# Kernel optimization log

Measured on AMD Instinct MI355X. Metric: run time of the kernel, lower is better.

Reference implementation:

```python
import jax, jax.numpy as jnp
import numpy as np

EMBED_DIM = 384
HIDDEN_DIM = 512
CODEBOOK_SIZE = 256
NUM_QUANTIZERS = 4
COMMIT_WEIGHT = 0.25
BATCH = 65536


def setup_inputs() -> dict:
    key = jax.random.key(0)
    ks = jax.random.split(key, 10)
    s_in = 1.0 / np.sqrt(EMBED_DIM)
    s_h = 1.0 / np.sqrt(HIDDEN_DIM)
    return {
        "x": jax.random.normal(ks[0], (BATCH, EMBED_DIM), jnp.float32),
        "enc_w1": jax.random.uniform(ks[1], (EMBED_DIM, HIDDEN_DIM), jnp.float32, -s_in, s_in),
        "enc_b1": jnp.zeros((HIDDEN_DIM,), jnp.float32),
        "enc_w2": jax.random.uniform(ks[2], (HIDDEN_DIM, HIDDEN_DIM), jnp.float32, -s_h, s_h),
        "enc_b2": jnp.zeros((HIDDEN_DIM,), jnp.float32),
        "codebooks": jax.random.normal(ks[3], (NUM_QUANTIZERS, CODEBOOK_SIZE, HIDDEN_DIM), jnp.float32),
        "dec_w1": jax.random.uniform(ks[4], (HIDDEN_DIM, HIDDEN_DIM), jnp.float32, -s_h, s_h),
        "dec_b1": jnp.zeros((HIDDEN_DIM,), jnp.float32),
        "dec_w2": jax.random.uniform(ks[5], (HIDDEN_DIM, EMBED_DIM), jnp.float32, -s_h, s_h),
        "dec_b2": jnp.zeros((EMBED_DIM,), jnp.float32),
    }


def _residual_vq(z, codebooks):
    """Sequential residual VQ with straight-through estimator and commitment loss.
    z: [B, D]; codebooks: [Q, K, D]. Returns quantized [B, D], indices [B, Q], commit_loss scalar."""
    residual = z
    quantized_out = jnp.zeros_like(z)
    commit_loss = jnp.asarray(0.0, z.dtype)
    idx_list = []
    for q in range(NUM_QUANTIZERS):
        cb = codebooks[q]  # [K, D]
        # nearest code: argmin ||r - c||^2 == argmax (2 r.c - ||c||^2)
        scores = 2.0 * (residual @ cb.T) - jnp.sum(cb * cb, axis=-1)  # [B, K]
        idx = jnp.argmax(scores, axis=-1)  # [B]
        quant = cb[idx]  # [B, D] gather
        commit_loss = commit_loss + COMMIT_WEIGHT * jnp.mean(
            (residual - jax.lax.stop_gradient(quant)) ** 2)
        # straight-through: value = quant, gradient flows to residual
        quant_st = residual + jax.lax.stop_gradient(quant - residual)
        quantized_out = quantized_out + quant_st
        residual = residual - jax.lax.stop_gradient(quant)
        idx_list.append(idx)
    indices = jnp.stack(idx_list, axis=-1)  # [B, Q]
    return quantized_out, indices, commit_loss


def reference(x, enc_w1, enc_b1, enc_w2, enc_b2, codebooks,
              dec_w1, dec_b1, dec_w2, dec_b2):
    # encoder MLP
    z = jax.nn.relu(x @ enc_w1 + enc_b1) @ enc_w2 + enc_b2  # [B, H]
    quantized, indices, commit_loss = _residual_vq(z, codebooks)
    # decoder MLP
    recon = jax.nn.relu(quantized @ dec_w1 + dec_b1) @ dec_w2 + dec_b2  # [B, E]
    recon_loss = jnp.mean((recon - x) ** 2)
    return recon, indices, recon_loss, commit_loss
```

## Files before the change

kernel.cpp:

```cpp
#include <hip/hip_runtime.h>
#include <cfloat>
#include <cstddef>
#include <cstdint>


#define BATCH   65536
#define EDIM    384
#define HDIM    512
#define NCODE   256
#define NQ      4

#define OUT_IDX_OFF 25165824
#define OUT_RL_OFF  25427968
#define WS_P0       0
#define WS_P1       33554432
#define WS_CBW      67108864
#define WS_CNORM    67633152
#define WS_COMMITP  67634176
#define WS_RECONP   67636224
#define WS_W1S      67637760
#define WS_W2S      67834368
#define WS_W3S      68096512
#define WS_W4S      68358656
#define WS_CBA      68555264
#define WS_G6       69079552
#define WS_ZN       69472768
#define WS_SSTAR    69538304
#define WS_IDXI     69800448

typedef _Float16 half8 __attribute__((ext_vector_type(8)));
typedef float    f32x16 __attribute__((ext_vector_type(16)));

__device__ __forceinline__ void cvt_hl8(const float* vs, half8& h, half8& l)
{
#pragma unroll
    for (int j = 0; j < 8; ++j) {
        _Float16 hv = (_Float16)vs[j];
        h[j] = hv;
        l[j] = (_Float16)(vs[j] - (float)hv);
    }
}

__device__ __forceinline__ void gll16(const unsigned short* g, unsigned short* l)
{
    __builtin_amdgcn_global_load_lds(
        (const __attribute__((address_space(1))) unsigned int*)g,
        (__attribute__((address_space(3))) unsigned int*)l, 16, 0, 0);
}

template <int N> __device__ __forceinline__ void waitvm()
{
    __builtin_amdgcn_sched_barrier(0);
    if constexpr (N == 0)      asm volatile("s_waitcnt vmcnt(0)" ::: "memory");
    else if constexpr (N == 6) asm volatile("s_waitcnt vmcnt(6)" ::: "memory");
    __builtin_amdgcn_sched_barrier(0);
}
__device__ __forceinline__ void barrier_raw()
{
    __builtin_amdgcn_s_barrier();
    __builtin_amdgcn_sched_barrier(0);
}

__global__ __launch_bounds__(256)
void split_act(const float* __restrict__ src, unsigned short* __restrict__ dst,
               int K)
{
    int u = blockIdx.x * 256 + threadIdx.x;
    int upr = K >> 3;
    int row = u / upr;
    int rem = u % upr;
    int kt = rem >> 1, kh = rem & 1;
    const float* p = src + (size_t)row * K + kt * 16 + kh * 8;
    float vs[8];
#pragma unroll
    for (int j = 0; j < 8; ++j) vs[j] = p[j];
    half8 h, l;
    cvt_hl8(vs, h, l);
    unsigned short* o = dst + (size_t)row * (2 * K) + kt * 32 + kh * 8;
    *reinterpret_cast<half8*>(o)      = h;
    *reinterpret_cast<half8*>(o + 16) = l;
}

__global__ __launch_bounds__(256)
void split_w(const float* __restrict__ W, unsigned short* __restrict__ out,
             int N, int K)
{
    int u = blockIdx.x * 256 + threadIdx.x;
    int col  = u % N;
    int rem  = u / N;
    int khalf = rem & 1;
    int kt    = rem >> 1;
    int kbase = kt * 16 + khalf * 8;
    float vs[8];
#pragma unroll
    for (int j = 0; j < 8; ++j) vs[j] = W[(size_t)(kbase + j) * N + col];
    half8 h, l;
    cvt_hl8(vs, h, l);
    *reinterpret_cast<half8*>(out + ((size_t)(kt * 4 + khalf) * N + col) * 8)     = h;
    *reinterpret_cast<half8*>(out + ((size_t)(kt * 4 + 2 + khalf) * N + col) * 8) = l;
}

__global__ __launch_bounds__(256)
void split_cbw(const float* __restrict__ cb, unsigned short* __restrict__ out)
{
    int u = blockIdx.x * 256 + threadIdx.x;
    int col = u & 1023;
    int rem = u >> 10;
    int kh = rem & 1;
    int kt = rem >> 1;
    const float* p = cb + (size_t)col * HDIM + kt * 16 + kh * 8;
    float vs[8];
#pragma unroll
    for (int j = 0; j < 8; ++j) vs[j] = p[j];
    half8 h, l;
    cvt_hl8(vs, h, l);
    *reinterpret_cast<half8*>(out + ((size_t)(kt * 4 + kh) * 1024 + col) * 8)     = h;
    *reinterpret_cast<half8*>(out + ((size_t)(kt * 4 + 2 + kh) * 1024 + col) * 8) = l;
}

__global__ __launch_bounds__(64)
void cnorm_kernel(const float* __restrict__ cb, float* __restrict__ cnorm)
{
    const int code = blockIdx.x;
    const int lane = threadIdx.x;
    const float* r = cb + (size_t)code * HDIM;
    float s = 0.f;
    for (int k = lane; k < HDIM; k += 64) s = fmaf(r[k], r[k], s);
#pragma unroll
    for (int off = 32; off > 0; off >>= 1) s += __shfl_down(s, off);
    if (lane == 0) cnorm[code] = s;
}

__global__ __launch_bounds__(256)
void rownorm(const unsigned short* __restrict__ zs, float* __restrict__ zn)
{
    const int tid = threadIdx.x, wid = tid >> 6, lane = tid & 63;
    const int row = blockIdx.x * 4 + wid;
    const unsigned short* p = zs + (size_t)row * 1024
                                 + (lane >> 1) * 32 + (lane & 1) * 8;
    half8 h = *reinterpret_cast<const half8*>(p);
    half8 l = *reinterpret_cast<const half8*>(p + 16);
    float s = 0.f;
#pragma unroll
    for (int e = 0; e < 8; ++e) {
        float v = (float)h[e] + (float)l[e];
        s = fmaf(v, v, s);
    }
#pragma unroll
    for (int off = 32; off > 0; off >>= 1) s += __shfl_down(s, off);
    if (lane == 0) zn[row] = s;
}

template <int BN, int NKT, int OMODE, bool RELU>
__global__ __launch_bounds__(256, 2)
void gemm_pl(const unsigned short* __restrict__ Ain,
             const unsigned short* __restrict__ Wsp,
             const float* __restrict__ bias, void* __restrict__ Cout,
             const float* __restrict__ X, float* __restrict__ lossP, int N)
{
    constexpr int WN  = BN / 128;
    constexpr int WM  = 4 / WN;
    constexpr int MR  = 128 / WM;
    constexpr int FM  = MR / 32;
    constexpr int K   = NKT * 16;
    constexpr int BOFF = 4096;
    constexpr int BUFU = 4096 + 4 * BN * 8;
    constexpr int NIB = BN / 64;

    __shared__ __align__(16) unsigned short lds[3][BUFU];

    const int tid  = threadIdx.x;
    const int wid  = tid >> 6;
    const int lane = tid & 63;
    const int l31  = lane & 31;
    const int lh   = lane >> 5;
    const int wm   = wid / WN;
    const int wn   = wid % WN;
    const int row0 = blockIdx.y * 128;
    const int n0   = blockIdx.x * BN;

    f32x16 acc[FM][4];
#pragma unroll
    for (int m = 0; m < FM; ++m)
#pragma unroll
        for (int n = 0; n < 4; ++n) acc[m][n] = (f32x16)(0.0f);

    auto stageB = [&](int buf, int kt) {
        const unsigned short* img = Wsp + (size_t)kt * 4 * N * 8;
        unsigned short* dstb = &lds[buf][BOFF];
#pragma unroll
        for (int t = 0; t < NIB; ++t) {
            int e = (wid * NIB + t) * 64 + lane;
            int u = (BN == 256) ? (e >> 8) : (e >> 7);
            int c = e & (BN - 1);
            gll16(img + ((size_t)u * N + n0 + c) * 8, dstb + (size_t)e * 8);
        }
    };
    auto stageA = [&](int buf, int kt) {
#pragma unroll
        for (int t = 0; t < 2; ++t) {
            int i = wid * 2 + t;
            int u = i >> 1, rh = i & 1;
            int row = rh * 64 + lane;
            gll16(Ain + (size_t)(row0 + row) * (2 * K) + kt * 32 + u * 8,
                  &lds[buf][(size_t)i * 512 + (size_t)lane * 8]);
        }
    };
    auto compute = [&](int buf) {
        const unsigned short* Ab = &lds[buf][0];
        const unsigned short* Bb = &lds[buf][BOFF];
        half8 Ah[FM], Al[FM];
#pragma unroll
        for (int fm = 0; fm < FM; ++fm) {
            int row = wm * MR + fm * 32 + l31;
            Ah[fm] = *reinterpret_cast<const half8*>(Ab + (size_t)lh * 1024 + (size_t)row * 8);
            Al[fm] = *reinterpret_cast<const half8*>(Ab + (size_t)(2 + lh) * 1024 + (size_t)row * 8);
        }
#pragma unroll
        for (int nt = 0; nt < 4; ++nt) {
            int col = wn * 128 + nt * 32 + l31;
            half8 Bh = *reinterpret_cast<const half8*>(Bb + (size_t)lh * BN * 8 + (size_t)col * 8);
            half8 Bl = *reinterpret_cast<const half8*>(Bb + (size_t)(2 + lh) * BN * 8 + (size_t)col * 8);
#pragma unroll
            for (int fm = 0; fm < FM; ++fm) {
                acc[fm][nt] = __builtin_amdgcn_mfma_f32_32x32x16_f16(Ah[fm], Bh, acc[fm][nt], 0, 0, 0);
                acc[fm][nt] = __builtin_amdgcn_mfma_f32_32x32x16_f16(Ah[fm], Bl, acc[fm][nt], 0, 0, 0);
                acc[fm][nt] = __builtin_amdgcn_mfma_f32_32x32x16_f16(Al[fm], Bh, acc[fm][nt], 0, 0, 0);
            }
        }
    };

    stageA(0, 0); stageB(0, 0);
    stageA(1, 1); stageB(1, 1);
    waitvm<6>();
    barrier_raw();
    for (int kt = 0; kt < NKT; ++kt) {
        const int cur = kt % 3;
        if (kt + 2 < NKT) { const int nb = (kt + 2) % 3; stageA(nb, kt + 2); stageB(nb, kt + 2); }
        compute(cur);
        if (kt < NKT - 2) waitvm<6>(); else waitvm<0>();
        barrier_raw();
    }

    if constexpr (OMODE == 0) {
        unsigned short* o = (unsigned short*)Cout;
        const size_t rs = (size_t)N * 2;
#pragma unroll
        for (int fm = 0; fm < FM; ++fm) {
#pragma unroll
            for (int nt = 0; nt < 4; ++nt) {
                const int col = n0 + wn * 128 + nt * 32 + l31;
                const float b = bias[col];
                const size_t cbo = (size_t)(col >> 4) * 32 + (size_t)((col >> 3) & 1) * 8 + (col & 7);
#pragma unroll
                for (int rg = 0; rg < 16; ++rg) {
                    const int row = row0 + wm * MR + fm * 32 + (rg & 3) + 8 * (rg >> 2) + 4 * lh;
                    float v = acc[fm][nt][rg] + b;
                    if (RELU) v = v > 0.f ? v : 0.f;
                    _Float16 hv = (_Float16)v;
                    _Float16 lv = (_Float16)(v - (float)hv);
                    union { _Float16 f; unsigned short u; } ch, cl;
                    ch.f = hv; cl.f = lv;
                    o[(size_t)row * rs + cbo]      = ch.u;
                    o[(size_t)row * rs + cbo + 16] = cl.u;
                }
            }
        }
    } else if constexpr (OMODE == 1) {
        float* C = (float*)Cout;
        float lacc = 0.f;
#pragma unroll
        for (int fm = 0; fm < FM; ++fm) {
#pragma unroll
            for (int nt = 0; nt < 4; ++nt) {
                const int col = n0 + wn * 128 + nt * 32 + l31;
                const float b = bias[col];
#pragma unroll
                for (int rg = 0; rg < 16; ++rg) {
                    const int row = row0 + wm * MR + fm * 32 + (rg & 3) + 8 * (rg >> 2) + 4 * lh;
                    float v = acc[fm][nt][rg] + b;
                    if (RELU) v = v > 0.f ? v : 0.f;
                    C[(size_t)row * N + col] = v;
                    float d = v - X[(size_t)row * N + col];
                    lacc = fmaf(d, d, lacc);
                }
            }
        }
        __shared__ float red[256];
        red[tid] = lacc;
        __syncthreads();
        for (int s = 128; s > 0; s >>= 1) {
            if (tid < s) red[tid] += red[tid + s];
            __syncthreads();
        }
        if (tid == 0) lossP[blockIdx.y * gridDim.x + blockIdx.x] = red[0];
    } else {
        float* C = (float*)Cout;
#pragma unroll
        for (int fm = 0; fm < FM; ++fm) {
#pragma unroll
            for (int nt = 0; nt < 4; ++nt) {
                const int col = wn * 128 + nt * 32 + l31;
#pragma unroll
                for (int rg = 0; rg < 16; ++rg) {
                    const int row = row0 + wm * MR + fm * 32 + (rg & 3) + 8 * (rg >> 2) + 4 * lh;
                    C[(size_t)row * 256 + col] = acc[fm][nt][rg];
                }
            }
        }
    }
}

template <int Q>
__global__ __launch_bounds__(256, 2)
void vq_score(const unsigned short* __restrict__ zs,
              const unsigned short* __restrict__ cbw,
              const float* __restrict__ G6,
              const float* __restrict__ cnorm,
              float* __restrict__ idx_out,
              int* __restrict__ idxi,
              float* __restrict__ sstar)
{
    constexpr int NKT = 32;
    constexpr int N   = 1024;
    __shared__ __align__(16) unsigned short lds[3][12288];
    __shared__ float sval[2][128];
    __shared__ int   sidx[2][128];

    const int tid  = threadIdx.x;
    const int wid  = tid >> 6;
    const int lane = tid & 63;
    const int l31  = lane & 31;
    const int lh   = lane >> 5;
    const int wm   = wid >> 1;
    const int wn   = wid & 1;
    const int row0 = blockIdx.x * 128;
    const int n0   = Q * 256;

    f32x16 acc[2][4];
#pragma unroll
    for (int m = 0; m < 2; ++m)
#pragma unroll
        for (int n = 0; n < 4; ++n) acc[m][n] = (f32x16)(0.0f);

    auto stageB = [&](int buf, int kt) {
        const unsigned short* img = cbw + (size_t)kt * 4 * N * 8;
        unsigned short* dstb = &lds[buf][4096];
#pragma unroll
        for (int t = 0; t < 4; ++t) {
            int e = (wid * 4 + t) * 64 + lane;
            int u = e >> 8;
            int c = e & 255;
            gll16(img + ((size_t)u * N + n0 + c) * 8, dstb + (size_t)e * 8);
        }
    };
    auto stageA = [&](int buf, int kt) {
#pragma unroll
        for (int t = 0; t < 2; ++t) {
            int i = wid * 2 + t;
            int u = i >> 1, rh = i & 1;
            int row = rh * 64 + lane;
            gll16(zs + (size_t)(row0 + row) * 1024 + kt * 32 + u * 8,
                  &lds[buf][(size_t)i * 512 + (size_t)lane * 8]);
        }
    };
    auto compute = [&](int buf) {
        const unsigned short* Ab = &lds[buf][0];
        const unsigned short* Bb = &lds[buf][4096];
        half8 Ah[2], Al[2];
#pragma unroll
        for (int fm = 0; fm < 2; ++fm) {
            int row = wm * 64 + fm * 32 + l31;
            Ah[fm] = *reinterpret_cast<const half8*>(Ab + (size_t)lh * 1024 + (size_t)row * 8);
            Al[fm] = *reinterpret_cast<const half8*>(Ab + (size_t)(2 + lh) * 1024 + (size_t)row * 8);
        }
#pragma unroll
        for (int nt = 0; nt < 4; ++nt) {
            int col = wn * 128 + nt * 32 + l31;
            half8 Bh = *reinterpret_cast<const half8*>(Bb + (size_t)lh * 2048 + (size_t)col * 8);
            half8 Bl = *reinterpret_cast<const half8*>(Bb + (size_t)(2 + lh) * 2048 + (size_t)col * 8);
#pragma unroll
            for (int fm = 0; fm < 2; ++fm) {
                acc[fm][nt] = __builtin_amdgcn_mfma_f32_32x32x16_f16(Ah[fm], Bh, acc[fm][nt], 0, 0, 0);
                acc[fm][nt] = __builtin_amdgcn_mfma_f32_32x32x16_f16(Ah[fm], Bl, acc[fm][nt], 0, 0, 0);
                acc[fm][nt] = __builtin_amdgcn_mfma_f32_32x32x16_f16(Al[fm], Bh, acc[fm][nt], 0, 0, 0);
            }
        }
    };

    stageA(0, 0); stageB(0, 0);
    stageA(1, 1); stageB(1, 1);
    waitvm<6>();
    barrier_raw();
    for (int kt = 0; kt < NKT; ++kt) {
        const int cur = kt % 3;
        if (kt + 2 < NKT) { const int nb = (kt + 2) % 3; stageA(nb, kt + 2); stageB(nb, kt + 2); }
        compute(cur);
        if (kt < NKT - 2) waitvm<6>(); else waitvm<0>();
        barrier_raw();
    }

    const float* cn = cnorm + Q * NCODE;
    constexpr int PAIR0 = (Q == 1) ? 0 : (Q == 2) ? 1 : 2;
    constexpr int PAIR1 = (Q == 2) ? 3 : 4;
    constexpr int PAIR2 = 5;
#pragma unroll
    for (int fm = 0; fm < 2; ++fm) {
#pragma unroll
        for (int rg = 0; rg < 16; ++rg) {
            const int grow = row0 + wm * 64 + fm * 32 + (rg & 3) + 8 * (rg >> 2) + 4 * lh;
            const float* gr0 = nullptr; const float* gr1 = nullptr; const float* gr2 = nullptr;
            if constexpr (Q > 0) gr0 = G6 + ((size_t)PAIR0 * 256 + idxi[0 * 65536 + grow]) * 256;
            if constexpr (Q > 1) gr1 = G6 + ((size_t)PAIR1 * 256 + idxi[1 * 65536 + grow]) * 256;
            if constexpr (Q > 2) gr2 = G6 + ((size_t)PAIR2 * 256 + idxi[2 * 65536 + grow]) * 256;
            float bv = -FLT_MAX;
            int   bi = 0;
#pragma unroll
            for (int nt = 0; nt < 4; ++nt) {
                const int code = wn * 128 + nt * 32 + l31;
                float a = acc[fm][nt][rg];
                if constexpr (Q > 0) a -= gr0[code];
                if constexpr (Q > 1) a -= gr1[code];
                if constexpr (Q > 2) a -= gr2[code];
                float s = 2.f * a - cn[code];
                if (s > bv || (s == bv && code < bi)) { bv = s; bi = code; }
            }
#pragma unroll
            for (int m = 1; m < 32; m <<= 1) {
                float ov = __shfl_xor(bv, m, 64);
                int   oi = __shfl_xor(bi, m, 64);
                if (ov > bv || (ov == bv && oi < bi)) { bv = ov; bi = oi; }
            }
            if (l31 == 0) {
                const int row = wm * 64 + fm * 32 + (rg & 3) + 8 * (rg >> 2) + 4 * lh;
                sval[wn][row] = bv;
                sidx[wn][row] = bi;
            }
        }
    }
    __syncthreads();
    if (tid < 128) {
        float v0 = sval[0][tid], v1 = sval[1][tid];
        int   i0 = sidx[0][tid], i1 = sidx[1][tid];
        float bv = (v1 > v0 || (v1 == v0 && i1 < i0)) ? v1 : v0;
        int   bi = (v1 > v0 || (v1 == v0 && i1 < i0)) ? i1 : i0;
        const int grow = row0 + tid;
        idxi[Q * 65536 + grow]  = bi;
        sstar[Q * 65536 + grow] = bv;
        idx_out[(size_t)grow * NQ + Q] = (float)bi;
    }
}

__global__ __launch_bounds__(256)
void vq_quant(const int* __restrict__ idxi, const float* __restrict__ sstar,
              const float* __restrict__ zn, const float* __restrict__ cb,
              unsigned short* __restrict__ qout, float* __restrict__ commitP)
{
    __shared__ float red[256];
    const int tid = threadIdx.x, wid = tid >> 6, lane = tid & 63;
    float ca = 0.f;

#pragma unroll
    for (int t = 0; t < 8; ++t) {
        const int row = blockIdx.x * 32 + wid * 8 + t;
        const int i0 = idxi[row],          i1 = idxi[65536 + row];
        const int i2 = idxi[131072 + row], i3 = idxi[196608 + row];
        const int koff = lane * 8;
        const float* c0 = cb + ((size_t)(0 * NCODE + i0)) * HDIM + koff;
        const float* c1 = cb + ((size_t)(1 * NCODE + i1)) * HDIM + koff;
        const float* c2 = cb + ((size_t)(2 * NCODE + i2)) * HDIM + koff;
        const float* c3 = cb + ((size_t)(3 * NCODE + i3)) * HDIM + koff;
        float q[8];
#pragma unroll
        for (int half = 0; half < 2; ++half) {
            float4 v0 = *reinterpret_cast<const float4*>(c0 + half * 4);
            float4 v1 = *reinterpret_cast<const float4*>(c1 + half * 4);
            float4 v2 = *reinterpret_cast<const float4*>(c2 + half * 4);
            float4 v3 = *reinterpret_cast<const float4*>(c3 + half * 4);
            q[half * 4 + 0] = ((v0.x + v1.x) + v2.x) + v3.x;
            q[half * 4 + 1] = ((v0.y + v1.y) + v2.y) + v3.y;
            q[half * 4 + 2] = ((v0.z + v1.z) + v2.z) + v3.z;
            q[half * 4 + 3] = ((v0.w + v1.w) + v2.w) + v3.w;
        }
        half8 oh, ol;
        cvt_hl8(q, oh, ol);
        unsigned short* op = qout + (size_t)row * 1024
                                  + (lane >> 1) * 32 + (lane & 1) * 8;
        *reinterpret_cast<half8*>(op)      = oh;
        *reinterpret_cast<half8*>(op + 16) = ol;

        if (lane == 0) {
            float rn = zn[row];
            rn -= sstar[row];           float cm = rn;
            rn -= sstar[65536 + row];   cm += rn;
            rn -= sstar[131072 + row];  cm += rn;
            rn -= sstar[196608 + row];  cm += rn;
            ca += cm;
        }
    }

    red[tid] = ca;
    __syncthreads();
    for (int s = 128; s > 0; s >>= 1) {
        if (tid < s) red[tid] += red[tid + s];
        __syncthreads();
    }
    if (tid == 0) commitP[blockIdx.x] = red[0];
}

__global__ __launch_bounds__(256)
void loss_reduce(const float* __restrict__ cP, int nc,
                 const float* __restrict__ rP, int nr,
                 float* __restrict__ out2)
{
    __shared__ float red[256];
    const int tid = threadIdx.x;

    float s = 0.f;
    for (int i = tid; i < nc; i += 256) s += cP[i];
    red[tid] = s;
    __syncthreads();
    for (int st = 128; st > 0; st >>= 1) {
        if (tid < st) red[tid] += red[tid + st];
        __syncthreads();
    }
    float ctot = red[0];
    __syncthreads();

    s = 0.f;
    for (int i = tid; i < nr; i += 256) s += rP[i];
    red[tid] = s;
    __syncthreads();
    for (int st = 128; st > 0; st >>= 1) {
        if (tid < st) red[tid] += red[tid + st];
        __syncthreads();
    }
    if (tid == 0) {
        out2[0] = red[0] / ((float)BATCH * (float)EDIM);
        out2[1] = 0.25f * ctot / ((float)BATCH * (float)HDIM);
    }
}

extern "C" void kernel_launch(void* const* d_in, const int* in_sizes, int n_in,
                              void* d_out, int out_size, void* d_ws, size_t ws_size,
                              hipStream_t stream)
{
    const float* x   = (const float*)d_in[0];
    const float* ew1 = (const float*)d_in[1];
    const float* eb1 = (const float*)d_in[2];
    const float* ew2 = (const float*)d_in[3];
    const float* eb2 = (const float*)d_in[4];
    const float* cb  = (const float*)d_in[5];
    const float* dw1 = (const float*)d_in[6];
    const float* db1 = (const float*)d_in[7];
    const float* dw2 = (const float*)d_in[8];
    const float* db2 = (const float*)d_in[9];

    float* out = (float*)d_out;
    float* ws  = (float*)d_ws;
    unsigned short* P0  = (unsigned short*)(ws + WS_P0);
    unsigned short* P1  = (unsigned short*)(ws + WS_P1);
    unsigned short* XS  = P1;
    unsigned short* cbw = (unsigned short*)(ws + WS_CBW);
    unsigned short* cba = (unsigned short*)(ws + WS_CBA);
    float* G6 = ws + WS_G6;
    float* zn = ws + WS_ZN;
    float* ss = ws + WS_SSTAR;
    int*   ii = (int*)(ws + WS_IDXI);
    float* cn = ws + WS_CNORM;
    float* cP = ws + WS_COMMITP;
    float* rP = ws + WS_RECONP;
    unsigned short* w1s = (unsigned short*)(ws + WS_W1S);
    unsigned short* w2s = (unsigned short*)(ws + WS_W2S);
    unsigned short* w3s = (unsigned short*)(ws + WS_W3S);
    unsigned short* w4s = (unsigned short*)(ws + WS_W4S);

    cnorm_kernel<<<NQ * NCODE, 64, 0, stream>>>(cb, cn);
    split_act<<<BATCH * 48 / 256, 256, 0, stream>>>(x, XS, EDIM);
    split_act<<<1024 * 64 / 256, 256, 0, stream>>>(cb, cba, HDIM);
    split_cbw<<<256, 256, 0, stream>>>(cb, cbw);
    split_w<<<(EDIM / 16) * 2 * HDIM / 256, 256, 0, stream>>>(ew1, w1s, HDIM, EDIM);
    split_w<<<(HDIM / 16) * 2 * HDIM / 256, 256, 0, stream>>>(ew2, w2s, HDIM, HDIM);
    split_w<<<(HDIM / 16) * 2 * HDIM / 256, 256, 0, stream>>>(dw1, w3s, HDIM, HDIM);
    split_w<<<(HDIM / 16) * 2 * EDIM / 256, 256, 0, stream>>>(dw2, w4s, EDIM, HDIM);

    {
        const int pairs[6][2] = {{0,1},{0,2},{0,3},{1,2},{1,3},{2,3}};
        for (int pi = 0; pi < 6; ++pi) {
            const int p = pairs[pi][0], q = pairs[pi][1];
            gemm_pl<256, 32, 2, false><<<dim3(1, 2), 256, 0, stream>>>(
                cba + (size_t)p * 256 * 1024, cbw + (size_t)q * 256 * 8,
                nullptr, G6 + (size_t)pi * 65536, nullptr, nullptr, 1024);
        }
    }

    gemm_pl<256, 24, 0, true><<<dim3(HDIM / 256, BATCH / 128), 256, 0, stream>>>(
        XS, w1s, eb1, P0, nullptr, nullptr, HDIM);
    gemm_pl<256, 32, 0, false><<<dim3(HDIM / 256, BATCH / 128), 256, 0, stream>>>(
        P0, w2s, eb2, P1, nullptr, nullptr, HDIM);

    rownorm<<<BATCH / 4, 256, 0, stream>>>(P1, zn);

    float* idxo = out + OUT_IDX_OFF;
    vq_score<0><<<BATCH / 128, 256, 0, stream>>>(P1, cbw, G6, cn, idxo, ii, ss);
    vq_score<1><<<BATCH / 128, 256, 0, stream>>>(P1, cbw, G6, cn, idxo, ii, ss);
    vq_score<2><<<BATCH / 128, 256, 0, stream>>>(P1, cbw, G6, cn, idxo, ii, ss);
    vq_score<3><<<BATCH / 128, 256, 0, stream>>>(P1, cbw, G6, cn, idxo, ii, ss);

    vq_quant<<<BATCH / 32, 256, 0, stream>>>(ii, ss, zn, cb, P0, cP);

    gemm_pl<256, 32, 0, true><<<dim3(HDIM / 256, BATCH / 128), 256, 0, stream>>>(
        P0, w3s, db1, P1, nullptr, nullptr, HDIM);
    gemm_pl<128, 32, 1, false><<<dim3(EDIM / 128, BATCH / 128), 256, 0, stream>>>(
        P1, w4s, db2, out, x, rP, EDIM);

    loss_reduce<<<1, 256, 0, stream>>>(cP, BATCH / 32, rP,
                                       (BATCH / 128) * (EDIM / 128),
                                       out + OUT_RL_OFF);
}
```

Before: 996.1 us.

## Compute all VQ scores in one GEMM, then run sequential argmax separately

Replaces the four per-quantizer fused score+argmax kernels with one GEMM of z against all 1024 codes, which writes fp32 scores to a workspace buffer. A lightweight kernel then does the sequential argmax per row, using precomputed codebook cross-Gram corrections. The batch is split into two halves so the score buffer fits in the workspace. The GEMM also gets a block-index swizzle across groups of eight workgroups, aimed at cache locality. The trade is extra global traffic for the score matrix (32768x1024 fp32 per half) in exchange for removing four separate GEMM passes and their repeated loads of A.

```diff
diff --git a/kernel.cpp b/kernel.cpp
--- a/kernel.cpp
+++ b/kernel.cpp
@@ -156,7 +156,8 @@
 void gemm_pl(const unsigned short* __restrict__ Ain,
              const unsigned short* __restrict__ Wsp,
              const float* __restrict__ bias, void* __restrict__ Cout,
-             const float* __restrict__ X, float* __restrict__ lossP, int N)
+             const float* __restrict__ X, float* __restrict__ lossP,
+             int N, int ldc)
 {
     constexpr int WN  = BN / 128;
     constexpr int WM  = 4 / WN;
@@ -176,8 +177,17 @@
     const int lh   = lane >> 5;
     const int wm   = wid / WN;
     const int wn   = wid % WN;
-    const int row0 = blockIdx.y * 128;
-    const int n0   = blockIdx.x * BN;
+
+    int bidx = blockIdx.y * gridDim.x + blockIdx.x;
+    const int nwg = gridDim.x * gridDim.y;
+    if ((nwg & 7) == 0) {
+        const int cpx = nwg >> 3;
+        bidx = (bidx & 7) * cpx + (bidx >> 3);
+    }
+    const int bx = bidx % gridDim.x;
+    const int by = bidx / gridDim.x;
+    const int row0 = by * 128;
+    const int n0   = bx * BN;
 
     f32x16 acc[FM][4];
 #pragma unroll
@@ -293,161 +303,85 @@
             if (tid < s) red[tid] += red[tid + s];
             __syncthreads();
         }
-        if (tid == 0) lossP[blockIdx.y * gridDim.x + blockIdx.x] = red[0];
+        if (tid == 0) lossP[by * gridDim.x + bx] = red[0];
     } else {
         float* C = (float*)Cout;
 #pragma unroll
         for (int fm = 0; fm < FM; ++fm) {
 #pragma unroll
             for (int nt = 0; nt < 4; ++nt) {
-                const int col = wn * 128 + nt * 32 + l31;
+                const int col = n0 + wn * 128 + nt * 32 + l31;
 #pragma unroll
                 for (int rg = 0; rg < 16; ++rg) {
                     const int row = row0 + wm * MR + fm * 32 + (rg & 3) + 8 * (rg >> 2) + 4 * lh;
-                    C[(size_t)row * 256 + col] = acc[fm][nt][rg];
+                    C[(size_t)row * ldc + col] = acc[fm][nt][rg];
                 }
             }
         }
     }
 }
 
-template <int Q>
-__global__ __launch_bounds__(256, 2)
-void vq_score(const unsigned short* __restrict__ zs,
-              const unsigned short* __restrict__ cbw,
-              const float* __restrict__ G6,
-              const float* __restrict__ cnorm,
-              float* __restrict__ idx_out,
-              int* __restrict__ idxi,
-              float* __restrict__ sstar)
-{
-    constexpr int NKT = 32;
-    constexpr int N   = 1024;
-    __shared__ __align__(16) unsigned short lds[3][12288];
-    __shared__ float sval[2][128];
-    __shared__ int   sidx[2][128];
-
-    const int tid  = threadIdx.x;
-    const int wid  = tid >> 6;
-    const int lane = tid & 63;
-    const int l31  = lane & 31;
-    const int lh   = lane >> 5;
-    const int wm   = wid >> 1;
-    const int wn   = wid & 1;
-    const int row0 = blockIdx.x * 128;
-    const int n0   = Q * 256;
-
-    f32x16 acc[2][4];
-#pragma unroll
-    for (int m = 0; m < 2; ++m)
-#pragma unroll
-        for (int n = 0; n < 4; ++n) acc[m][n] = (f32x16)(0.0f);
-
-    auto stageB = [&](int buf, int kt) {
-        const unsigned short* img = cbw + (size_t)kt * 4 * N * 8;
-        unsigned short* dstb = &lds[buf][4096];
-#pragma unroll
-        for (int t = 0; t < 4; ++t) {
-            int e = (wid * 4 + t) * 64 + lane;
-            int u = e >> 8;
-            int c = e & 255;
-            gll16(img + ((size_t)u * N + n0 + c) * 8, dstb + (size_t)e * 8);
-        }
-    };
-    auto stageA = [&](int buf, int kt) {
-#pragma unroll
-        for (int t = 0; t < 2; ++t) {
-            int i = wid * 2 + t;
-            int u = i >> 1, rh = i & 1;
-            int row = rh * 64 + lane;
-            gll16(zs + (size_t)(row0 + row) * 1024 + kt * 32 + u * 8,
-                  &lds[buf][(size_t)i * 512 + (size_t)lane * 8]);
-        }
-    };
-    auto compute = [&](int buf) {
-        const unsigned short* Ab = &lds[buf][0];
-        const unsigned short* Bb = &lds[buf][4096];
-        half8 Ah[2], Al[2];
-#pragma unroll
-        for (int fm = 0; fm < 2; ++fm) {
-            int row = wm * 64 + fm * 32 + l31;
-            Ah[fm] = *reinterpret_cast<const half8*>(Ab + (size_t)lh * 1024 + (size_t)row * 8);
-            Al[fm] = *reinterpret_cast<const half8*>(Ab + (size_t)(2 + lh) * 1024 + (size_t)row * 8);
-        }
-#pragma unroll
-        for (int nt = 0; nt < 4; ++nt) {
-            int col = wn * 128 + nt * 32 + l31;
-            half8 Bh = *reinterpret_cast<const half8*>(Bb + (size_t)lh * 2048 + (size_t)col * 8);
-            half8 Bl = *reinterpret_cast<const half8*>(Bb + (size_t)(2 + lh) * 2048 + (size_t)col * 8);
-#pragma unroll
-            for (int fm = 0; fm < 2; ++fm) {
-                acc[fm][nt] = __builtin_amdgcn_mfma_f32_32x32x16_f16(Ah[fm], Bh, acc[fm][nt], 0, 0, 0);
-                acc[fm][nt] = __builtin_amdgcn_mfma_f32_32x32x16_f16(Ah[fm], Bl, acc[fm][nt], 0, 0, 0);
-                acc[fm][nt] = __builtin_amdgcn_mfma_f32_32x32x16_f16(Al[fm], Bh, acc[fm][nt], 0, 0, 0);
-            }
-        }
-    };
-
-    stageA(0, 0); stageB(0, 0);
-    stageA(1, 1); stageB(1, 1);
-    waitvm<6>();
-    barrier_raw();
-    for (int kt = 0; kt < NKT; ++kt) {
-        const int cur = kt % 3;
-        if (kt + 2 < NKT) { const int nb = (kt + 2) % 3; stageA(nb, kt + 2); stageB(nb, kt + 2); }
-        compute(cur);
-        if (kt < NKT - 2) waitvm<6>(); else waitvm<0>();
-        barrier_raw();
-    }
-
-    const float* cn = cnorm + Q * NCODE;
-    constexpr int PAIR0 = (Q == 1) ? 0 : (Q == 2) ? 1 : 2;
-    constexpr int PAIR1 = (Q == 2) ? 3 : 4;
-    constexpr int PAIR2 = 5;
-#pragma unroll
-    for (int fm = 0; fm < 2; ++fm) {
-#pragma unroll
-        for (int rg = 0; rg < 16; ++rg) {
-            const int grow = row0 + wm * 64 + fm * 32 + (rg & 3) + 8 * (rg >> 2) + 4 * lh;
-            const float* gr0 = nullptr; const float* gr1 = nullptr; const float* gr2 = nullptr;
-            if constexpr (Q > 0) gr0 = G6 + ((size_t)PAIR0 * 256 + idxi[0 * 65536 + grow]) * 256;
-            if constexpr (Q > 1) gr1 = G6 + ((size_t)PAIR1 * 256 + idxi[1 * 65536 + grow]) * 256;
-            if constexpr (Q > 2) gr2 = G6 + ((size_t)PAIR2 * 256 + idxi[2 * 65536 + grow]) * 256;
-            float bv = -FLT_MAX;
-            int   bi = 0;
-#pragma unroll
-            for (int nt = 0; nt < 4; ++nt) {
-                const int code = wn * 128 + nt * 32 + l31;
-                float a = acc[fm][nt][rg];
-                if constexpr (Q > 0) a -= gr0[code];
-                if constexpr (Q > 1) a -= gr1[code];
-                if constexpr (Q > 2) a -= gr2[code];
-                float s = 2.f * a - cn[code];
-                if (s > bv || (s == bv && code < bi)) { bv = s; bi = code; }
-            }
-#pragma unroll
-            for (int m = 1; m < 32; m <<= 1) {
-                float ov = __shfl_xor(bv, m, 64);
-                int   oi = __shfl_xor(bi, m, 64);
-                if (ov > bv || (ov == bv && oi < bi)) { bv = ov; bi = oi; }
-            }
-            if (l31 == 0) {
-                const int row = wm * 64 + fm * 32 + (rg & 3) + 8 * (rg >> 2) + 4 * lh;
-                sval[wn][row] = bv;
-                sidx[wn][row] = bi;
-            }
-        }
-    }
-    __syncthreads();
-    if (tid < 128) {
-        float v0 = sval[0][tid], v1 = sval[1][tid];
-        int   i0 = sidx[0][tid], i1 = sidx[1][tid];
-        float bv = (v1 > v0 || (v1 == v0 && i1 < i0)) ? v1 : v0;
-        int   bi = (v1 > v0 || (v1 == v0 && i1 < i0)) ? i1 : i0;
-        const int grow = row0 + tid;
-        idxi[Q * 65536 + grow]  = bi;
-        sstar[Q * 65536 + grow] = bv;
-        idx_out[(size_t)grow * NQ + Q] = (float)bi;
+__global__ __launch_bounds__(256)
+void vq_argmax(const float* __restrict__ S,
+               const float* __restrict__ G6,
+               const float* __restrict__ cnorm,
+               float* __restrict__ idx_out,
+               int* __restrict__ idxi,
+               float* __restrict__ sstar,
+               int rowbase)
+{
+    const int tid = threadIdx.x, wid = tid >> 6, lane = tid & 63;
+    const int lrow = blockIdx.x * 4 + wid;
+    const int grow = rowbase + lrow;
+    const float* srow = S + (size_t)lrow * 1024;
+    const int c0 = lane * 4;
+
+    int iprev0 = 0, iprev1 = 0, iprev2 = 0;
+
+#pragma unroll
+    for (int q = 0; q < NQ; ++q) {
+        float4 sv = *reinterpret_cast<const float4*>(srow + q * 256 + c0);
+        float a[4] = {sv.x, sv.y, sv.z, sv.w};
+        if (q >= 1) {
+            const float* g = G6 + ((size_t)(q - 1) * 256 + iprev0) * 256 + c0;
+            float4 gv = *reinterpret_cast<const float4*>(g);
+            a[0] -= gv.x; a[1] -= gv.y; a[2] -= gv.z; a[3] -= gv.w;
+        }
+        if (q >= 2) {
+            const float* g = G6 + ((size_t)(q + 1) * 256 + iprev1) * 256 + c0;
+            float4 gv = *reinterpret_cast<const float4*>(g);
+            a[0] -= gv.x; a[1] -= gv.y; a[2] -= gv.z; a[3] -= gv.w;
+        }
+        if (q >= 3) {
+            const float* g = G6 + ((size_t)5 * 256 + iprev2) * 256 + c0;
+            float4 gv = *reinterpret_cast<const float4*>(g);
+            a[0] -= gv.x; a[1] -= gv.y; a[2] -= gv.z; a[3] -= gv.w;
+        }
+        float4 cnv = *reinterpret_cast<const float4*>(cnorm + q * 256 + c0);
+        float cna[4] = {cnv.x, cnv.y, cnv.z, cnv.w};
+
+        float bv = -FLT_MAX;
+        int   bi = 0;
+#pragma unroll
+        for (int j = 0; j < 4; ++j) {
+            float s = 2.f * a[j] - cna[j];
+            const int code = c0 + j;
+            if (s > bv || (s == bv && code < bi)) { bv = s; bi = code; }
+        }
+#pragma unroll
+        for (int m = 1; m < 64; m <<= 1) {
+            float ov = __shfl_xor(bv, m, 64);
+            int   oi = __shfl_xor(bi, m, 64);
+            if (ov > bv || (ov == bv && oi < bi)) { bv = ov; bi = oi; }
+        }
+        if (q == 0) iprev0 = bi;
+        else if (q == 1) iprev1 = bi;
+        else if (q == 2) iprev2 = bi;
+        if (lane == 0) {
+            idxi[q * 65536 + grow]  = bi;
+            sstar[q * 65536 + grow] = bv;
+            idx_out[(size_t)grow * NQ + q] = (float)bi;
+        }
     }
 }
 
@@ -561,6 +495,7 @@
     unsigned short* P0  = (unsigned short*)(ws + WS_P0);
     unsigned short* P1  = (unsigned short*)(ws + WS_P1);
     unsigned short* XS  = P1;
+    float* Sbuf = ws + WS_P0;
     unsigned short* cbw = (unsigned short*)(ws + WS_CBW);
     unsigned short* cba = (unsigned short*)(ws + WS_CBA);
     float* G6 = ws + WS_G6;
@@ -590,29 +525,32 @@
             const int p = pairs[pi][0], q = pairs[pi][1];
             gemm_pl<256, 32, 2, false><<<dim3(1, 2), 256, 0, stream>>>(
                 cba + (size_t)p * 256 * 1024, cbw + (size_t)q * 256 * 8,
-                nullptr, G6 + (size_t)pi * 65536, nullptr, nullptr, 1024);
+                nullptr, G6 + (size_t)pi * 65536, nullptr, nullptr, 1024, 256);
         }
     }
 
     gemm_pl<256, 24, 0, true><<<dim3(HDIM / 256, BATCH / 128), 256, 0, stream>>>(
-        XS, w1s, eb1, P0, nullptr, nullptr, HDIM);
+        XS, w1s, eb1, P0, nullptr, nullptr, HDIM, HDIM);
     gemm_pl<256, 32, 0, false><<<dim3(HDIM / 256, BATCH / 128), 256, 0, stream>>>(
-        P0, w2s, eb2, P1, nullptr, nullptr, HDIM);
+        P0, w2s, eb2, P1, nullptr, nullptr, HDIM, HDIM);
 
     rownorm<<<BATCH / 4, 256, 0, stream>>>(P1, zn);
 
     float* idxo = out + OUT_IDX_OFF;
-    vq_score<0><<<BATCH / 128, 256, 0, stream>>>(P1, cbw, G6, cn, idxo, ii, ss);
-    vq_score<1><<<BATCH / 128, 256, 0, stream>>>(P1, cbw, G6, cn, idxo, ii, ss);
-    vq_score<2><<<BATCH / 128, 256, 0, stream>>>(P1, cbw, G6, cn, idxo, ii, ss);
-    vq_score<3><<<BATCH / 128, 256, 0, stream>>>(P1, cbw, G6, cn, idxo, ii, ss);
+    for (int half = 0; half < 2; ++half) {
+        const int rowbase = half * 32768;
+        gemm_pl<256, 32, 2, false><<<dim3(4, 256), 256, 0, stream>>>(
+            P1 + (size_t)rowbase * 1024, cbw, nullptr, Sbuf,
+            nullptr, nullptr, 1024, 1024);
+        vq_argmax<<<8192, 256, 0, stream>>>(Sbuf, G6, cn, idxo, ii, ss, rowbase);
+    }
 
     vq_quant<<<BATCH / 32, 256, 0, stream>>>(ii, ss, zn, cb, P0, cP);
 
     gemm_pl<256, 32, 0, true><<<dim3(HDIM / 256, BATCH / 128), 256, 0, stream>>>(
-        P0, w3s, db1, P1, nullptr, nullptr, HDIM);
+        P0, w3s, db1, P1, nullptr, nullptr, HDIM, HDIM);
     gemm_pl<128, 32, 1, false><<<dim3(EDIM / 128, BATCH / 128), 256, 0, stream>>>(
-        P1, w4s, db2, out, x, rP, EDIM);
+        P1, w4s, db2, out, x, rP, EDIM, EDIM);
 
     loss_reduce<<<1, 256, 0, stream>>>(cP, BATCH / 32, rP,
                                        (BATCH / 128) * (EDIM / 128),
```

Result: faster. 968.7 us (-2.7%).
